# Optimization experiments

Hardware: AMD Instinct MI355X
Metric: run time of the kernel (lower is better)

Reference implementation:

```python
import jax, jax.numpy as jnp
import numpy as np

N_NODES = 50000
N_EDGES = 800000
X_DIM, EDGE_DIM, H_DIM, HOUT = 92, 80, 128, 128
N_CONV = 3
N_GRAPHS = 256
BN_EPS = 1e-5


def setup_inputs() -> dict:
    key = jax.random.key(0)
    ks = jax.random.split(key, 16)
    x = jax.random.normal(ks[0], (N_NODES, X_DIM), dtype=jnp.float32)
    edge_index = jax.random.randint(ks[1], (2, N_EDGES), 0, N_NODES, dtype=jnp.int64)
    edge_attr = jax.random.normal(ks[2], (N_EDGES, EDGE_DIM), dtype=jnp.float32)
    batch = jnp.sort(jax.random.randint(ks[3], (N_NODES,), 0, N_GRAPHS, dtype=jnp.int64))
    s = 0.05
    embed_W = jax.random.normal(ks[4], (X_DIM, H_DIM), dtype=jnp.float32) * s
    embed_b = jnp.zeros((H_DIM,), jnp.float32)
    in_dim = 2 * H_DIM + EDGE_DIM
    conv_W = jax.random.normal(ks[5], (N_CONV, in_dim, 2 * H_DIM), dtype=jnp.float32) * s
    conv_b = jnp.zeros((N_CONV, 2 * H_DIM), jnp.float32)
    bn_i_g = jnp.ones((N_CONV, 2 * H_DIM), jnp.float32)
    bn_i_b = jnp.zeros((N_CONV, 2 * H_DIM), jnp.float32)
    bn_o_g = jnp.ones((N_CONV, H_DIM), jnp.float32)
    bn_o_b = jnp.zeros((N_CONV, H_DIM), jnp.float32)
    lin_W = jax.random.normal(ks[6], (H_DIM, HOUT), dtype=jnp.float32) * s
    lin_b = jnp.zeros((HOUT,), jnp.float32)
    out_W = jax.random.normal(ks[7], (HOUT, 1), dtype=jnp.float32) * s
    out_b = jnp.zeros((1,), jnp.float32)
    return {"x": x, "edge_index": edge_index, "edge_attr": edge_attr, "batch": batch,
            "embed_W": embed_W, "embed_b": embed_b, "conv_W": conv_W, "conv_b": conv_b,
            "bn_i_g": bn_i_g, "bn_i_b": bn_i_b, "bn_o_g": bn_o_g, "bn_o_b": bn_o_b,
            "lin_W": lin_W, "lin_b": lin_b, "out_W": out_W, "out_b": out_b}


def _bn(h, gamma, beta):
    # training-mode BatchNorm1d: biased batch statistics
    mu = jnp.mean(h, axis=0)
    var = jnp.mean(jnp.square(h - mu), axis=0)
    return (h - mu) * jax.lax.rsqrt(var + BN_EPS) * gamma + beta


def _cgconv(x, edge_index, edge_attr, W, b, gi, bi, go, bo):
    src, dst = edge_index[0], edge_index[1]
    msg = jnp.concatenate([x[src], edge_attr, x[dst]], axis=1)  # [E, 2h+e]
    msg = msg @ W + b                                           # [E, 2h]
    msg = _bn(msg, gi, bi)
    filt, core = jnp.split(msg, 2, axis=1)
    gated = jax.nn.sigmoid(filt) * jax.nn.softplus(core)        # [E, h]
    agg = jax.ops.segment_sum(gated, src, num_segments=N_NODES)  # [N, h]
    agg = _bn(agg, go, bo)
    return jax.nn.softplus(x + agg)


def reference(x, edge_index, edge_attr, batch, embed_W, embed_b, conv_W, conv_b,
              bn_i_g, bn_i_b, bn_o_g, bn_o_b, lin_W, lin_b, out_W, out_b):
    h = x @ embed_W + embed_b  # [N, h_dim]
    for i in range(N_CONV):
        h = _cgconv(h, edge_index, edge_attr, conv_W[i], conv_b[i],
                    bn_i_g[i], bn_i_b[i], bn_o_g[i], bn_o_b[i])
    # mean pooling per graph
    sums = jax.ops.segment_sum(h, batch, num_segments=N_GRAPHS)
    cnts = jax.ops.segment_sum(jnp.ones((h.shape[0],), h.dtype), batch, num_segments=N_GRAPHS)
    pooled = sums / jnp.maximum(cnts, 1.0)[:, None]  # [G, h_dim]
    g = jax.nn.softplus(pooled @ lin_W + lin_b)
    return g @ out_W + out_b  # [G, 1]
```

## Files before the change

### kernel.cpp

```cpp
#include <hip/hip_runtime.h>

constexpr int NN = 50000;
constexpr int NE = 800000;
constexpr int XD = 92;
constexpr int ED = 80;
constexpr int HD = 128;
constexpr int C2 = 256;
constexpr int IND = 336;
constexpr int NC = 3;
constexpr int NG = 256;
constexpr int NTILES = NE / 64;
constexpr int WSZ_L = 16 * 3 * 64 * 8;
constexpr int WNP_L = 16 * 4 * 64 * 8;

#define DINL __device__ __forceinline__

typedef __attribute__((ext_vector_type(8))) short bf16x8;
typedef __attribute__((ext_vector_type(4))) float f32x4;

DINL short f2bf(float f) {
  unsigned u = __float_as_uint(f);
  u = (u + 0x7fffu + ((u >> 16) & 1u)) >> 16;
  return (short)u;
}
DINL float bf2f(unsigned short u) { return __uint_as_float(((unsigned)u) << 16); }
DINL float bflo(unsigned u) { return __uint_as_float(u << 16); }
DINL float bfhi(unsigned u) { return __uint_as_float(u & 0xffff0000u); }
DINL float rcp_(float x) {
  float r;
  asm("v_rcp_f32 %0, %1" : "=v"(r) : "v"(x));
  return r;
}
DINL float softplusf_(float x) { return x > 20.f ? x : log1pf(__expf(x)); }
DINL float gate_(float f, float cr) {
  float e = __expf(-f);
  float s = rcp_(1.f + e);
  float t = __expf(cr);
  float l = (cr > 15.f) ? cr : __logf(1.f + t);
  return s * l;
}

template <int CTRL>
DINL int dpp_i(int old_, int src) {
  return __builtin_amdgcn_update_dpp(old_, src, CTRL, 0xF, 0xF, false);
}
template <int CTRL>
DINL float dpp_f(float old_, float src) {
  return __int_as_float(
      __builtin_amdgcn_update_dpp(__float_as_int(old_), __float_as_int(src), CTRL, 0xF, 0xF, false));
}
constexpr int SHR1 = 0x111, SHR2 = 0x112, SHR4 = 0x114, SHR8 = 0x118, SHL1 = 0x101;

__global__ __launch_bounds__(256) void k_embed(const float* __restrict__ x,
    const float* __restrict__ W, const float* __restrict__ b, float* __restrict__ h,
    unsigned short* __restrict__ hbf) {
  __shared__ float xs[2][XD];
  int t = threadIdx.x;
  int n0 = blockIdx.x * 2;
  for (int i = t; i < 2 * XD; i += 256) xs[i / XD][i % XD] = x[(size_t)n0 * XD + i];
  __syncthreads();
  int lo = t >> 7, c = t & 127;
  float acc = b[c];
  for (int k = 0; k < XD; ++k) acc = fmaf(xs[lo][k], W[k * HD + c], acc);
  h[(size_t)(n0 + lo) * HD + c] = acc;
  hbf[(size_t)(n0 + lo) * HD + c] = (unsigned short)f2bf(acc);
}

__global__ __launch_bounds__(256) void k_hist(const int* __restrict__ src,
                                              int* __restrict__ deg) {
  for (int e = blockIdx.x * 256 + threadIdx.x; e < NE; e += gridDim.x * 256)
    atomicAdd(&deg[src[e]], 1);
}

__global__ __launch_bounds__(1024) void k_scan(const int* __restrict__ deg,
                                               int* __restrict__ cursor) {
  __shared__ int sums[1024];
  int t = threadIdx.x;
  const int CH = 49;
  int b0 = t * CH;
  int s = 0;
  for (int i = 0; i < CH; ++i) {
    int idx = b0 + i;
    if (idx < NN) s += deg[idx];
  }
  sums[t] = s;
  __syncthreads();
  for (int off = 1; off < 1024; off <<= 1) {
    int v = (t >= off) ? sums[t - off] : 0;
    __syncthreads();
    sums[t] += v;
    __syncthreads();
  }
  int excl = (t == 0) ? 0 : sums[t - 1];
  for (int i = 0; i < CH; ++i) {
    int idx = b0 + i;
    if (idx < NN) {
      cursor[idx] = excl;
      excl += deg[idx];
    }
  }
}

__global__ __launch_bounds__(256) void k_scatter(const int* __restrict__ src,
    const int* __restrict__ dst, int* __restrict__ cursor, int* __restrict__ eid,
    int* __restrict__ ssort, int* __restrict__ dsort) {
  for (int e = blockIdx.x * 256 + threadIdx.x; e < NE; e += gridDim.x * 256) {
    int s = src[e];
    int pos = atomicAdd(&cursor[s], 1);
    eid[pos] = e;
    ssort[pos] = s;
    dsort[pos] = dst[e];
  }
}

__global__ __launch_bounds__(256) void k_wprep(const float* __restrict__ convW,
                                               unsigned short* __restrict__ Wswz) {
  int idx = blockIdx.x * 256 + threadIdx.x;
  if (idx >= NC * WSZ_L) return;
  int L = idx / WSZ_L;
  int rem = idx - L * WSZ_L;
  int mt = rem / 1536;
  int rem2 = rem - mt * 1536;
  int ks = rem2 >> 9;
  int lane = (rem2 >> 3) & 63;
  int j = rem2 & 7;
  int k = ks * 32 + (lane >> 4) * 8 + j;
  int m = mt * 16 + (lane & 15);
  float v = (k < ED) ? convW[(size_t)L * IND * C2 + (size_t)(HD + k) * C2 + m] : 0.f;
  Wswz[idx] = (unsigned short)f2bf(v);
}

__global__ __launch_bounds__(256) void k_wprep2(const float* __restrict__ convW,
                                                unsigned short* __restrict__ Wn) {
  int idx = blockIdx.x * 256 + threadIdx.x;
  if (idx >= NC * 2 * WNP_L) return;
  int Lh = idx >> 15;
  int L = Lh >> 1, half = Lh & 1;
  int rem = idx & 32767;
  int mt = rem >> 11;
  int rem2 = rem & 2047;
  int ks = rem2 >> 9;
  int lane = (rem2 >> 3) & 63;
  int j = rem2 & 7;
  int k = ks * 32 + (lane >> 4) * 8 + j;
  int m = mt * 16 + (lane & 15);
  int row = (half ? 208 : 0) + k;
  Wn[idx] = (unsigned short)f2bf(convW[(size_t)L * IND * C2 + (size_t)row * C2 + m]);
}

__global__ __launch_bounds__(256) void k_nodeproj2(const unsigned short* __restrict__ hbf,
    const unsigned short* __restrict__ Wn, int L,
    ushort4* __restrict__ P1, ushort4* __restrict__ P3) {
  __shared__ bf16x8 hls[1024];
  __shared__ ushort4 outls[4096];
  int t = threadIdx.x, w = t >> 6, l = t & 63, g = l >> 4, c = l & 15;
  int n0 = blockIdx.x * 64;
  int half = blockIdx.y;
  for (int i = t; i < 1024; i += 256) {
    int node = i >> 4, chunk = i & 15;
    int gn = n0 + node;
    if (gn >= NN) gn = NN - 1;
    bf16x8 v = *(const bf16x8*)(hbf + (size_t)gn * HD + chunk * 8);
    hls[node * 16 + (chunk ^ (node & 7))] = v;
  }
  __syncthreads();
  const bf16x8* Wf = (const bf16x8*)(Wn + ((size_t)(L * 2 + half)) * WNP_L);
  bf16x8 af[4][4];
#pragma unroll
  for (int mm = 0; mm < 4; ++mm)
#pragma unroll
    for (int ks = 0; ks < 4; ++ks) af[mm][ks] = Wf[((w * 4 + mm) * 4 + ks) * 64 + l];
  f32x4 acc[4][4];
#pragma unroll
  for (int mm = 0; mm < 4; ++mm)
#pragma unroll
    for (int nt = 0; nt < 4; ++nt)
#pragma unroll
      for (int i = 0; i < 4; ++i) acc[mm][nt][i] = 0.f;
#pragma unroll
  for (int nt = 0; nt < 4; ++nt) {
    int node = nt * 16 + c;
#pragma unroll
    for (int ks = 0; ks < 4; ++ks) {
      bf16x8 b = hls[node * 16 + ((4 * ks + g) ^ (node & 7))];
#pragma unroll
      for (int mm = 0; mm < 4; ++mm)
        acc[mm][nt] = __builtin_amdgcn_mfma_f32_16x16x32_bf16(af[mm][ks], b, acc[mm][nt], 0, 0, 0);
    }
  }
  __syncthreads();
#pragma unroll
  for (int mm = 0; mm < 4; ++mm) {
    int mt = w * 4 + mm;
    int wE = (mt & 7) >> 1;
    int mE = (mt & 1) | ((mt >> 3) << 1);
    int slot = (wE * 4 + g) * 4 + mE;
#pragma unroll
    for (int nt = 0; nt < 4; ++nt) {
      int node = nt * 16 + c;
      ushort4 st;
      st.x = (unsigned short)f2bf(acc[mm][nt][0]);
      st.y = (unsigned short)f2bf(acc[mm][nt][1]);
      st.z = (unsigned short)f2bf(acc[mm][nt][2]);
      st.w = (unsigned short)f2bf(acc[mm][nt][3]);
      outls[node * 64 + (slot ^ ((node & 7) << 3))] = st;
    }
  }
  __syncthreads();
  ushort4* P = half ? P3 : P1;
  for (int i = t; i < 4096; i += 256) {
    int row = i >> 6, slot = i & 63;
    int gn = n0 + row;
    if (gn < NN) P[(size_t)gn * 64 + slot] = outls[row * 64 + (slot ^ ((row & 7) << 3))];
  }
}

__global__ __launch_bounds__(256) void k_eaprep(const int* __restrict__ eid,
    const float* __restrict__ ea, bf16x8* __restrict__ eaf) {
  int idx = blockIdx.x * 256 + threadIdx.x;
  if (idx >= NTILES * 768) return;
  int tile = idx / 768;
  int r = idx - tile * 768;
  int fr = r >> 6, l = r & 63;
  int nt = fr / 3, ks = fr - 3 * nt;
  int c = l & 15, g = l >> 4;
  int k0 = ks * 32 + g * 8;
  bf16x8 v;
  if (k0 < ED) {
    int e = eid[tile * 64 + nt * 16 + c];
    const float* p = ea + (size_t)e * ED + k0;
    float4 x0 = *(const float4*)p;
    float4 x1 = *(const float4*)(p + 4);
    v[0] = f2bf(x0.x); v[1] = f2bf(x0.y); v[2] = f2bf(x0.z); v[3] = f2bf(x0.w);
    v[4] = f2bf(x1.x); v[5] = f2bf(x1.y); v[6] = f2bf(x1.z); v[7] = f2bf(x1.w);
  } else {
#pragma unroll
    for (int j = 0; j < 8; ++j) v[j] = 0;
  }
  eaf[idx] = v;
}

__global__ __launch_bounds__(256, 2) void k_estat2(
    const int* __restrict__ ssort, const int* __restrict__ dsort,
    const bf16x8* __restrict__ eaf, const unsigned short* __restrict__ Wswz,
    const uint4* __restrict__ P1p, const uint4* __restrict__ P3p,
    ushort4* __restrict__ msgc, float* __restrict__ stats) {
  int t = threadIdx.x;
  int w = t >> 6, l = t & 63;
  int g = l >> 4, c = l & 15;
  int mtg[4] = {2 * w, 2 * w + 1, 2 * w + 8, 2 * w + 9};
  int gi2 = (w * 4 + g) * 2;
  const bf16x8* Wf = (const bf16x8*)Wswz;
  bf16x8 af[4][3];
#pragma unroll
  for (int m = 0; m < 4; ++m)
#pragma unroll
    for (int ks = 0; ks < 3; ++ks) af[m][ks] = Wf[(mtg[m] * 3 + ks) * 64 + l];
  f32x4 ssum[4], ssq[4];
#pragma unroll
  for (int m = 0; m < 4; ++m)
#pragma unroll
    for (int i = 0; i < 4; ++i) { ssum[m][i] = 0.f; ssq[m][i] = 0.f; }

  const int stride = gridDim.x;
  int tile = blockIdx.x;
  int s_[4], d_[4];
  if (tile < NTILES) {
#pragma unroll
    for (int nt = 0; nt < 4; ++nt) {
      s_[nt] = ssort[tile * 64 + nt * 16 + c];
      d_[nt] = dsort[tile * 64 + nt * 16 + c];
    }
  }
  for (; tile < NTILES; tile += stride) {
    bf16x8 b_[12];
    const bf16x8* bp = eaf + (size_t)tile * 768 + l;
#pragma unroll
    for (int fr = 0; fr < 12; ++fr) b_[fr] = bp[fr * 64];
    uint4 q1a[4], q1b[4], q3a[4], q3b[4];
#pragma unroll
    for (int nt = 0; nt < 4; ++nt) {
      const uint4* p1 = P1p + (size_t)s_[nt] * 32 + gi2;
      const uint4* p3 = P3p + (size_t)d_[nt] * 32 + gi2;
      q1a[nt] = p1[0];
      q1b[nt] = p1[1];
      q3a[nt] = p3[0];
      q3b[nt] = p3[1];
    }
    int sn[4], dn[4];
    int tn = tile + stride;
    if (tn < NTILES) {
#pragma unroll
      for (int nt = 0; nt < 4; ++nt) {
        sn[nt] = ssort[tn * 64 + nt * 16 + c];
        dn[nt] = dsort[tn * 64 + nt * 16 + c];
      }
    } else {
#pragma unroll
      for (int nt = 0; nt < 4; ++nt) { sn[nt] = 0; dn[nt] = 0; }
    }
#pragma unroll
    for (int nt = 0; nt < 4; ++nt) {
      f32x4 acc[4];
#pragma unroll
      for (int m = 0; m < 4; ++m) {
        acc[m][0] = 0.f; acc[m][1] = 0.f; acc[m][2] = 0.f; acc[m][3] = 0.f;
      }
#pragma unroll
      for (int ks = 0; ks < 3; ++ks)
#pragma unroll
        for (int m = 0; m < 4; ++m)
          acc[m] = __builtin_amdgcn_mfma_f32_16x16x32_bf16(af[m][ks], b_[nt * 3 + ks],
                                                           acc[m], 0, 0, 0);
      unsigned pu1[8] = {q1a[nt].x, q1a[nt].y, q1a[nt].z, q1a[nt].w,
                         q1b[nt].x, q1b[nt].y, q1b[nt].z, q1b[nt].w};
      unsigned pu3[8] = {q3a[nt].x, q3a[nt].y, q3a[nt].z, q3a[nt].w,
                         q3b[nt].x, q3b[nt].y, q3b[nt].z, q3b[nt].w};
#pragma unroll
      for (int m = 0; m < 4; ++m) {
        unsigned a1 = pu1[2 * m], b1 = pu1[2 * m + 1];
        unsigned a3 = pu3[2 * m], b3 = pu3[2 * m + 1];
        f32x4 ms;
        ms[0] = acc[m][0] + bflo(a1) + bflo(a3);
        ms[1] = acc[m][1] + bfhi(a1) + bfhi(a3);
        ms[2] = acc[m][2] + bflo(b1) + bflo(b3);
        ms[3] = acc[m][3] + bfhi(b1) + bfhi(b3);
#pragma unroll
        for (int i = 0; i < 4; ++i) {
          ssum[m][i] += ms[i];
          ssq[m][i] = fmaf(ms[i], ms[i], ssq[m][i]);
        }
        ushort4 st;
        st.x = (unsigned short)f2bf(ms[0]);
        st.y = (unsigned short)f2bf(ms[1]);
        st.z = (unsigned short)f2bf(ms[2]);
        st.w = (unsigned short)f2bf(ms[3]);
        msgc[(((size_t)tile * 4 + nt) * 16 + w * 4 + m) * 64 + l] = st;
      }
    }
#pragma unroll
    for (int nt = 0; nt < 4; ++nt) { s_[nt] = sn[nt]; d_[nt] = dn[nt]; }
  }
#pragma unroll
  for (int off = 1; off < 16; off <<= 1)
#pragma unroll
    for (int m = 0; m < 4; ++m)
#pragma unroll
      for (int i = 0; i < 4; ++i) {
        ssum[m][i] += __shfl_xor(ssum[m][i], off, 16);
        ssq[m][i] += __shfl_xor(ssq[m][i], off, 16);
      }
  if (c == 0) {
#pragma unroll
    for (int m = 0; m < 4; ++m)
#pragma unroll
      for (int i = 0; i < 4; ++i) {
        int ch = mtg[m] * 16 + 4 * g + i;
        atomicAdd(&stats[ch], ssum[m][i]);
        atomicAdd(&stats[C2 + ch], ssq[m][i]);
      }
  }
}

__global__ __launch_bounds__(256) void k_apply2(
    const int* __restrict__ ssort, const ushort4* __restrict__ msgc,
    const float* __restrict__ st, const float* __restrict__ gammaI,
    const float* __restrict__ betaI, float* __restrict__ agg) {
  int t = threadIdx.x;
  int w = t >> 6, l = t & 63;
  int g = l >> 4, c = l & 15;
  int mtg[4] = {2 * w, 2 * w + 1, 2 * w + 8, 2 * w + 9};
  f32x4 sc4[4], sh4[4];
#pragma unroll
  for (int m = 0; m < 4; ++m)
#pragma unroll
    for (int i = 0; i < 4; ++i) {
      int ch = mtg[m] * 16 + 4 * g + i;
      float mean = st[ch] * (1.f / NE);
      float var = st[C2 + ch] * (1.f / NE) - mean * mean;
      float scv = gammaI[ch] * rsqrtf(var + 1e-5f);
      sc4[m][i] = scv;
      sh4[m][i] = betaI[ch] - mean * scv;
    }
  for (int tile = blockIdx.x; tile < NTILES; tile += gridDim.x) {
    int e0 = tile * 64;
    int s_[4];
#pragma unroll
    for (int nt = 0; nt < 4; ++nt) s_[nt] = ssort[e0 + nt * 16 + c];
    ushort4 mw[4][4];
#pragma unroll
    for (int nt = 0; nt < 4; ++nt)
#pragma unroll
      for (int m = 0; m < 4; ++m)
        mw[nt][m] = msgc[(((size_t)tile * 4 + nt) * 16 + w * 4 + m) * 64 + l];
#pragma unroll
    for (int nt = 0; nt < 4; ++nt) {
      int sv = s_[nt];
      int ps = dpp_i<SHR1>(-1, sv);
      int hp = (ps != sv) ? c : 0;
      hp = max(hp, dpp_i<SHR1>(0, hp));
      hp = max(hp, dpp_i<SHR2>(0, hp));
      hp = max(hp, dpp_i<SHR4>(0, hp));
      hp = max(hp, dpp_i<SHR8>(0, hp));
      int ns = dpp_i<SHL1>(-1, sv);
      bool tail = (ns != sv);
      bool g1 = (c - 1) >= hp, g2 = (c - 2) >= hp, g4 = (c - 4) >= hp, g8 = (c - 8) >= hp;
      f32x4 v4[4];
#pragma unroll
      for (int m = 0; m < 4; ++m) {
        v4[m][0] = fmaf(bf2f(mw[nt][m].x), sc4[m][0], sh4[m][0]);
        v4[m][1] = fmaf(bf2f(mw[nt][m].y), sc4[m][1], sh4[m][1]);
        v4[m][2] = fmaf(bf2f(mw[nt][m].z), sc4[m][2], sh4[m][2]);
        v4[m][3] = fmaf(bf2f(mw[nt][m].w), sc4[m][3], sh4[m][3]);
      }
      float gg_[8];
#pragma unroll
      for (int p = 0; p < 2; ++p)
#pragma unroll
        for (int i = 0; i < 4; ++i)
          gg_[p * 4 + i] = gate_(v4[p][i], v4[p + 2][i]);
#pragma unroll
      for (int q = 0; q < 8; ++q) {
        float tv;
        tv = dpp_f<SHR1>(0.f, gg_[q]); gg_[q] += g1 ? tv : 0.f;
        tv = dpp_f<SHR2>(0.f, gg_[q]); gg_[q] += g2 ? tv : 0.f;
        tv = dpp_f<SHR4>(0.f, gg_[q]); gg_[q] += g4 ? tv : 0.f;
        tv = dpp_f<SHR8>(0.f, gg_[q]); gg_[q] += g8 ? tv : 0.f;
      }
      if (tail) {
#pragma unroll
        for (int p = 0; p < 2; ++p)
#pragma unroll
          for (int i = 0; i < 4; ++i)
            atomicAdd(&agg[(size_t)sv * HD + mtg[p] * 16 + 4 * g + i], gg_[p * 4 + i]);
      }
    }
  }
}

__global__ __launch_bounds__(256) void k_aggstat(const float* __restrict__ agg,
                                                 float* __restrict__ stats) {
  int t = threadIdx.x;
  int c = t & 127, half = t >> 7;
  float s = 0.f, sq = 0.f;
  for (int n = blockIdx.x * 2 + half; n < NN; n += gridDim.x * 2) {
    float v = agg[(size_t)n * HD + c];
    s += v;
    sq = fmaf(v, v, sq);
  }
  __shared__ float shs[2][128], shq[2][128];
  shs[half][c] = s;
  shq[half][c] = sq;
  __syncthreads();
  if (t < 128) {
    atomicAdd(&stats[c], shs[0][c] + shs[1][c]);
    atomicAdd(&stats[128 + c], shq[0][c] + shq[1][c]);
  }
}

__global__ __launch_bounds__(256) void k_update(const float* __restrict__ h,
    const float* __restrict__ agg, const float* __restrict__ st_o,
    const float* __restrict__ bog, const float* __restrict__ bob,
    float* __restrict__ hn, unsigned short* __restrict__ hbf) {
  int stride = gridDim.x * 256;
  for (int i = blockIdx.x * 256 + threadIdx.x; i < NN * HD; i += stride) {
    int c = i & 127;
    float mean = st_o[c] * (1.f / NN);
    float var = st_o[128 + c] * (1.f / NN) - mean * mean;
    float scv = bog[c] * rsqrtf(var + 1e-5f);
    float shv = bob[c] - mean * scv;
    float v = h[i] + fmaf(agg[i], scv, shv);
    float r = softplusf_(v);
    hn[i] = r;
    hbf[i] = (unsigned short)f2bf(r);
  }
}

__global__ __launch_bounds__(256) void k_pool(const float* __restrict__ h,
    const int* __restrict__ batch, float* __restrict__ psum, int* __restrict__ pcnt) {
  int stride = gridDim.x * 256;
  for (int i = blockIdx.x * 256 + threadIdx.x; i < NN * HD; i += stride) {
    int n = i >> 7, c = i & 127;
    int g = batch[n];
    atomicAdd(&psum[g * HD + c], h[i]);
    if (c == 0) atomicAdd(&pcnt[g], 1);
  }
}

__global__ __launch_bounds__(128) void k_head(const float* __restrict__ psum,
    const int* __restrict__ pcnt, const float* __restrict__ linW,
    const float* __restrict__ linb, const float* __restrict__ outW,
    const float* __restrict__ outb, float* __restrict__ out) {
  __shared__ float pl[HD];
  __shared__ float red[2];
  int g = blockIdx.x, t = threadIdx.x;
  float cnt = fmaxf((float)pcnt[g], 1.f);
  pl[t] = psum[g * HD + t] / cnt;
  __syncthreads();
  float acc = linb[t];
  for (int k = 0; k < HD; ++k) acc = fmaf(pl[k], linW[k * HD + t], acc);
  float term = softplusf_(acc) * outW[t];
#pragma unroll
  for (int off = 32; off > 0; off >>= 1) term += __shfl_down(term, off, 64);
  if ((t & 63) == 0) red[t >> 6] = term;
  __syncthreads();
  if (t == 0) out[g] = red[0] + red[1] + outb[0];
}

extern "C" void kernel_launch(void* const* d_in, const int* in_sizes, int n_in,
                              void* d_out, int out_size, void* d_ws, size_t ws_size,
                              hipStream_t stream) {
  const float* x = (const float*)d_in[0];
  const int* ei = (const int*)d_in[1];
  const float* ea = (const float*)d_in[2];
  const int* batch = (const int*)d_in[3];
  const float* embW = (const float*)d_in[4];
  const float* embb = (const float*)d_in[5];
  const float* convW = (const float*)d_in[6];
  const float* big = (const float*)d_in[8];
  const float* bib = (const float*)d_in[9];
  const float* bog = (const float*)d_in[10];
  const float* bob = (const float*)d_in[11];
  const float* linW = (const float*)d_in[12];
  const float* linb = (const float*)d_in[13];
  const float* outW = (const float*)d_in[14];
  const float* outb = (const float*)d_in[15];
  float* out = (float*)d_out;

  float* wsf = (float*)d_ws;
  size_t off = 0;
  auto alloc = [&](size_t n) {
    float* p = wsf + off;
    off += (n + 3) & ~(size_t)3;
    return p;
  };
  float* h0 = alloc((size_t)NN * HD);
  float* h1 = alloc((size_t)NN * HD);
  unsigned short* hbf = (unsigned short*)alloc((size_t)NN * HD / 2);
  ushort4* P1b = (ushort4*)alloc((size_t)NN * C2 / 2);
  ushort4* P3b = (ushort4*)alloc((size_t)NN * C2 / 2);
  float* agg = alloc((size_t)NN * HD);
  float* st_i = alloc(2 * C2);
  float* st_o = alloc(2 * HD);
  float* psum = alloc((size_t)NG * HD);
  int* pcnt = (int*)alloc(NG);
  int* deg = (int*)alloc(NN);
  int* cursor = (int*)alloc(NN);
  int* eid = (int*)alloc(NE);
  int* ssort = (int*)alloc(NE);
  int* dsort = (int*)alloc(NE);
  unsigned short* Wswz = (unsigned short*)alloc((NC * WSZ_L + 1) / 2);
  unsigned short* Wn = (unsigned short*)alloc((NC * 2 * WNP_L + 1) / 2);
  bf16x8* eaf = (bf16x8*)alloc((size_t)NTILES * 768 * 4);
  ushort4* msgc = (ushort4*)alloc((size_t)NE * C2 / 2);

  const int* srcp = ei;
  const int* dstp = ei + NE;

  hipMemsetAsync(deg, 0, NN * sizeof(int), stream);
  k_hist<<<2048, 256, 0, stream>>>(srcp, deg);
  k_scan<<<1, 1024, 0, stream>>>(deg, cursor);
  k_scatter<<<2048, 256, 0, stream>>>(srcp, dstp, cursor, eid, ssort, dsort);

  k_wprep<<<(NC * WSZ_L + 255) / 256, 256, 0, stream>>>(convW, Wswz);
  k_wprep2<<<(NC * 2 * WNP_L + 255) / 256, 256, 0, stream>>>(convW, Wn);
  k_eaprep<<<(NTILES * 768 + 255) / 256, 256, 0, stream>>>(eid, ea, eaf);
  k_embed<<<NN / 2, 256, 0, stream>>>(x, embW, embb, h0, hbf);

  float* hc = h0;
  float* hn = h1;
  for (int L = 0; L < NC; ++L) {
    const unsigned short* Wl = Wswz + (size_t)L * WSZ_L;
    hipMemsetAsync(st_i, 0, 2 * C2 * sizeof(float), stream);
    hipMemsetAsync(st_o, 0, 2 * HD * sizeof(float), stream);
    hipMemsetAsync(agg, 0, (size_t)NN * HD * sizeof(float), stream);

    dim3 npgrid((NN + 63) / 64, 2);
    k_nodeproj2<<<npgrid, 256, 0, stream>>>(hbf, Wn, L, P1b, P3b);
    k_estat2<<<2500, 256, 0, stream>>>(ssort, dsort, eaf, Wl,
        (const uint4*)P1b, (const uint4*)P3b, msgc, st_i);
    k_apply2<<<2500, 256, 0, stream>>>(ssort, msgc, st_i, big + L * C2, bib + L * C2, agg);
    k_aggstat<<<512, 256, 0, stream>>>(agg, st_o);
    k_update<<<2048, 256, 0, stream>>>(hc, agg, st_o, bog + L * HD, bob + L * HD, hn, hbf);
    float* tmp = hc; hc = hn; hn = tmp;
  }

  hipMemsetAsync(psum, 0, (size_t)NG * HD * sizeof(float), stream);
  hipMemsetAsync(pcnt, 0, NG * sizeof(int), stream);
  k_pool<<<2048, 256, 0, stream>>>(hc, batch, psum, pcnt);
  k_head<<<NG, 128, 0, stream>>>(psum, pcnt, linW, linb, outW, outb, out);
}
```

Baseline: 2.248 ms.

## Use contiguous tile ranges and prefetch next edge-attr tile in estat kernel

Switches k_estat2 from grid-strided tiles to a contiguous chunk of tiles per block and cuts the grid from 2500 to 512 blocks. Edge-attribute fragments for the next tile are loaded into registers while the current tile runs its MFMAs (double buffering). This aims to hide global load latency and to spread the stats atomics over fewer blocks. In exchange it adds 12 more vector registers per lane, which may lower occupancy, and the last tile issues a wasted reload of the first tile.

```diff
diff --git a/kernel.cpp b/kernel.cpp
--- a/kernel.cpp
+++ b/kernel.cpp
@@ -262,21 +262,27 @@
 #pragma unroll
     for (int i = 0; i < 4; ++i) { ssum[m][i] = 0.f; ssq[m][i] = 0.f; }
 
-  const int stride = gridDim.x;
-  int tile = blockIdx.x;
+  int nblk = gridDim.x;
+  int per = (NTILES + nblk - 1) / nblk;
+  int t0 = blockIdx.x * per;
+  int t1 = min(t0 + per, NTILES);
+  if (t0 >= NTILES) return;
+
   int s_[4], d_[4];
-  if (tile < NTILES) {
-#pragma unroll
-    for (int nt = 0; nt < 4; ++nt) {
-      s_[nt] = ssort[tile * 64 + nt * 16 + c];
-      d_[nt] = dsort[tile * 64 + nt * 16 + c];
-    }
-  }
-  for (; tile < NTILES; tile += stride) {
-    bf16x8 b_[12];
-    const bf16x8* bp = eaf + (size_t)tile * 768 + l;
-#pragma unroll
-    for (int fr = 0; fr < 12; ++fr) b_[fr] = bp[fr * 64];
+  bf16x8 bcur[12];
+#pragma unroll
+  for (int nt = 0; nt < 4; ++nt) {
+    s_[nt] = ssort[t0 * 64 + nt * 16 + c];
+    d_[nt] = dsort[t0 * 64 + nt * 16 + c];
+  }
+  {
+    const bf16x8* bp = eaf + (size_t)t0 * 768 + l;
+#pragma unroll
+    for (int fr = 0; fr < 12; ++fr) bcur[fr] = bp[fr * 64];
+  }
+  for (int tile = t0; tile < t1; ++tile) {
+    int tn = tile + 1;
+    bool more = (tn < t1);
     uint4 q1a[4], q1b[4], q3a[4], q3b[4];
 #pragma unroll
     for (int nt = 0; nt < 4; ++nt) {
@@ -288,16 +294,17 @@
       q3b[nt] = p3[1];
     }
     int sn[4], dn[4];
-    int tn = tile + stride;
-    if (tn < NTILES) {
-#pragma unroll
-      for (int nt = 0; nt < 4; ++nt) {
-        sn[nt] = ssort[tn * 64 + nt * 16 + c];
-        dn[nt] = dsort[tn * 64 + nt * 16 + c];
-      }
-    } else {
-#pragma unroll
-      for (int nt = 0; nt < 4; ++nt) { sn[nt] = 0; dn[nt] = 0; }
+    int ti = more ? tn : t0;
+#pragma unroll
+    for (int nt = 0; nt < 4; ++nt) {
+      sn[nt] = ssort[ti * 64 + nt * 16 + c];
+      dn[nt] = dsort[ti * 64 + nt * 16 + c];
+    }
+    bf16x8 bnext[12];
+    {
+      const bf16x8* bp = eaf + (size_t)ti * 768 + l;
+#pragma unroll
+      for (int fr = 0; fr < 12; ++fr) bnext[fr] = bp[fr * 64];
     }
 #pragma unroll
     for (int nt = 0; nt < 4; ++nt) {
@@ -310,7 +317,7 @@
       for (int ks = 0; ks < 3; ++ks)
 #pragma unroll
         for (int m = 0; m < 4; ++m)
-          acc[m] = __builtin_amdgcn_mfma_f32_16x16x32_bf16(af[m][ks], b_[nt * 3 + ks],
+          acc[m] = __builtin_amdgcn_mfma_f32_16x16x32_bf16(af[m][ks], bcur[nt * 3 + ks],
                                                            acc[m], 0, 0, 0);
       unsigned pu1[8] = {q1a[nt].x, q1a[nt].y, q1a[nt].z, q1a[nt].w,
                          q1b[nt].x, q1b[nt].y, q1b[nt].z, q1b[nt].w};
@@ -340,6 +347,8 @@
     }
 #pragma unroll
     for (int nt = 0; nt < 4; ++nt) { s_[nt] = sn[nt]; d_[nt] = dn[nt]; }
+#pragma unroll
+    for (int fr = 0; fr < 12; ++fr) bcur[fr] = bnext[fr];
   }
 #pragma unroll
   for (int off = 1; off < 16; off <<= 1)
@@ -577,7 +586,7 @@
 
     dim3 npgrid((NN + 63) / 64, 2);
     k_nodeproj2<<<npgrid, 256, 0, stream>>>(hbf, Wn, L, P1b, P3b);
-    k_estat2<<<2500, 256, 0, stream>>>(ssort, dsort, eaf, Wl,
+    k_estat2<<<512, 256, 0, stream>>>(ssort, dsort, eaf, Wl,
         (const uint4*)P1b, (const uint4*)P3b, msgc, st_i);
     k_apply2<<<2500, 256, 0, stream>>>(ssort, msgc, st_i, big + L * C2, bib + L * C2, agg);
     k_aggstat<<<512, 256, 0, stream>>>(agg, st_o);
```

Result: slower. 2.423 ms (+7.8%).
